# Performance work log

Measured on AMD Instinct MI355X. Metric: run time of the kernel, lower is better.

The kernel has to match this reference:

```python
import jax, jax.numpy as jnp
import numpy as np
import math

IN_DIM, ATTN_DIM, OUT_DIM, NUM_HEADS = 64, 128, 64, 4
B, N = 32, 1024


def setup_inputs() -> dict:
    key = jax.random.key(0)
    ks = jax.random.split(key, 8)
    def glorot(k, fan_in, fan_out):
        s = math.sqrt(6.0 / (fan_in + fan_out))
        return jax.random.uniform(k, (fan_in, fan_out), jnp.float32, -s, s)
    return {
        "x": jax.random.normal(ks[0], (B, N, IN_DIM), jnp.float32),
        "adj": jax.random.uniform(ks[1], (B, N, N), jnp.float32),
        "flags": jnp.ones((B, N), jnp.float32),
        "Wq": glorot(ks[2], IN_DIM, ATTN_DIM), "bq": jnp.zeros((ATTN_DIM,), jnp.float32),
        "Wk": glorot(ks[3], IN_DIM, ATTN_DIM), "bk": jnp.zeros((ATTN_DIM,), jnp.float32),
        "Wv": glorot(ks[4], IN_DIM, OUT_DIM), "bv": jnp.zeros((OUT_DIM,), jnp.float32),
    }


def dense_gcn(x, adj, W, b):
    # add self-loops (improved=False -> diagonal set to 1)
    n = adj.shape[-1]
    idx = jnp.arange(n)
    adj = adj.at[:, idx, idx].set(1.0)
    h = x @ W                                   # [B,N,C_out]
    d = jnp.clip(adj.sum(-1), 1.0) ** -0.5      # [B,N]
    adj_n = d[:, :, None] * adj * d[:, None, :]
    return adj_n @ h + b


def reference(x, adj, flags, Wq, bq, Wk, bk, Wv, bv):
    del flags  # accepted but unused by the original forward
    Q = dense_gcn(x, adj, Wq, bq)               # [B,N,attn]
    K = dense_gcn(x, adj, Wk, bk)               # [B,N,attn]
    V = dense_gcn(x, adj, Wv, bv)               # [B,N,out]
    dh = ATTN_DIM // NUM_HEADS
    b_, n_ = adj.shape[0], adj.shape[1]
    # torch.cat(split(dh,-1), dim=0) == heads as leading axis
    Q_ = Q.reshape(b_, n_, NUM_HEADS, dh).transpose(2, 0, 1, 3)  # [H,B,N,dh]
    K_ = K.reshape(b_, n_, NUM_HEADS, dh).transpose(2, 0, 1, 3)
    scores = jnp.einsum('hbnd,hbmd->hbnm', Q_, K_) / math.sqrt(OUT_DIM)
    A = jnp.tanh(scores)                        # [H,B,N,N]
    A = A.mean(axis=0)                          # [B,N,N]
    A = (A + A.transpose(0, 2, 1)) * 0.5        # symmetrize
    return V, A
```

## Files before the change

kernel.cpp:

```cpp
#include <hip/hip_runtime.h>
#include <stdint.h>

typedef __attribute__((ext_vector_type(4))) float f32x4;
typedef __attribute__((ext_vector_type(4))) unsigned int u32x4;
typedef __attribute__((ext_vector_type(2))) unsigned int u32x2;
typedef __attribute__((ext_vector_type(8))) short bf16x8;

__device__ __forceinline__ unsigned short f2bf(float f) {
    union { float f; unsigned int u; } c; c.f = f;
    unsigned int u = c.u;
    unsigned int r = (u + 0x7FFFu + ((u >> 16) & 1u)) >> 16;
    return (unsigned short)r;
}
__device__ __forceinline__ float bf2f(unsigned short h) {
    union { unsigned int u; float f; } c; c.u = ((unsigned int)h) << 16;
    return c.f;
}
__device__ __forceinline__ float tanh_fast(float x) {
    float t = __expf(2.0f * x);
    return 1.0f - 2.0f * __builtin_amdgcn_rcpf(t + 1.0f);
}

__global__ __launch_bounds__(256) void k_deg(const float* __restrict__ adj,
                                             float* __restrict__ dvec) {
    int wid = threadIdx.x >> 6, l = threadIdx.x & 63;
    int row = blockIdx.x * 4 + wid;
    int b = row >> 10, i = row & 1023;
    const float* rp = adj + ((size_t)b << 20) + ((size_t)i << 10);
    float s = 0.f;
#pragma unroll
    for (int it = 0; it < 4; ++it) {
        f32x4 v = *(const f32x4*)(rp + it * 256 + l * 4);
        s += v.x + v.y + v.z + v.w;
    }
#pragma unroll
    for (int m = 32; m >= 1; m >>= 1) s += __shfl_xor(s, m);
    if (l == 0) {
        float diag = rp[i];
        float S = s - diag + 1.0f;
        S = fmaxf(S, 1.0f);
        dvec[(b << 10) + i] = 1.0f / sqrtf(S);
    }
}

__global__ __launch_bounds__(256) void k_xs(const float* __restrict__ x,
                                            const float* __restrict__ dvec,
                                            unsigned short* __restrict__ xsT) {
    __shared__ float Lt[64][65];
    int b = blockIdx.x >> 4, j0 = (blockIdx.x & 15) << 6;
    int tid = threadIdx.x;
    {
        int r = tid >> 2, cseg = (tid & 3) << 4;
        float dj = dvec[(b << 10) + j0 + r];
        const float* xr = x + (((size_t)((b << 10) + j0 + r)) << 6) + cseg;
#pragma unroll
        for (int q = 0; q < 4; ++q) {
            f32x4 v = *(const f32x4*)(xr + (q << 2));
#pragma unroll
            for (int e = 0; e < 4; ++e) Lt[r][cseg + (q << 2) + e] = v[e] * dj;
        }
    }
    __syncthreads();
    {
        int c = tid >> 2, js = (tid & 3) << 4;
        unsigned int pk[8];
#pragma unroll
        for (int e = 0; e < 8; ++e) {
            unsigned short lo16 = f2bf(Lt[js + 2 * e][c]);
            unsigned short hi16 = f2bf(Lt[js + 2 * e + 1][c]);
            pk[e] = (unsigned)lo16 | ((unsigned)hi16 << 16);
        }
        unsigned short* op = xsT + ((size_t)b << 16) + ((size_t)c << 10) + j0 + js;
        u32x4 w0 = {pk[0], pk[1], pk[2], pk[3]};
        u32x4 w1 = {pk[4], pk[5], pk[6], pk[7]};
        *(u32x4*)op = w0;
        *(u32x4*)(op + 8) = w1;
    }
}

#define APAD 72
__global__ __launch_bounds__(256) void k_m(const float* __restrict__ adj,
                                           const unsigned short* __restrict__ xsT,
                                           const float* __restrict__ dvec,
                                           float* __restrict__ Mg) {
    __shared__ unsigned short Al[32][APAD];
    __shared__ unsigned short Bl[64][APAD];
    int bid = blockIdx.x;
    int xcd = bid & 7, t2 = bid >> 3;
    int bg = t2 >> 5, mt = t2 & 31;
    int b = (bg << 3) + xcd;
    int i0 = mt << 5;
    int tid = threadIdx.x;
    int wid = tid >> 6, l = tid & 63;
    int wm = wid >> 1, wn = wid & 1;
    int lr = l & 15, lg = l >> 4;

    f32x4 acc[2];
    acc[0] = (f32x4){0.f, 0.f, 0.f, 0.f};
    acc[1] = (f32x4){0.f, 0.f, 0.f, 0.f};

    const float* adjB = adj + ((size_t)b << 20);
    const unsigned short* xsB = xsT + ((size_t)b << 16);
    int ar0 = tid >> 4;
    int ac4 = (tid & 15) << 2;

    for (int kt = 0; kt < 16; ++kt) {
        int j0 = kt << 6;
        __syncthreads();
#pragma unroll
        for (int rr = 0; rr < 2; ++rr) {
            int row = ar0 + (rr << 4);
            int gi  = i0 + row;
            f32x4 v = *(const f32x4*)(adjB + ((size_t)gi << 10) + j0 + ac4);
            int gj = j0 + ac4;
            if (gj + 0 == gi) v.x = 1.0f;
            if (gj + 1 == gi) v.y = 1.0f;
            if (gj + 2 == gi) v.z = 1.0f;
            if (gj + 3 == gi) v.w = 1.0f;
            u32x2 pk;
            pk.x = (unsigned)f2bf(v.x) | ((unsigned)f2bf(v.y) << 16);
            pk.y = (unsigned)f2bf(v.z) | ((unsigned)f2bf(v.w) << 16);
            *(u32x2*)&Al[row][ac4] = pk;
        }
#pragma unroll
        for (int rep = 0; rep < 2; ++rep) {
            int idx = (rep << 8) + tid;
            int crow = idx >> 3, ch = (idx & 7) << 3;
            u32x4 v = *(const u32x4*)(xsB + ((size_t)crow << 10) + j0 + ch);
            *(u32x4*)&Bl[crow][ch] = v;
        }
        __syncthreads();
#pragma unroll
        for (int kk = 0; kk < 2; ++kk) {
            bf16x8 av = *(const bf16x8*)&Al[wm * 16 + lr][kk * 32 + lg * 8];
            bf16x8 b0 = *(const bf16x8*)&Bl[wn * 32 + lr][kk * 32 + lg * 8];
            bf16x8 b1 = *(const bf16x8*)&Bl[wn * 32 + 16 + lr][kk * 32 + lg * 8];
            acc[0] = __builtin_amdgcn_mfma_f32_16x16x32_bf16(av, b0, acc[0], 0, 0, 0);
            acc[1] = __builtin_amdgcn_mfma_f32_16x16x32_bf16(av, b1, acc[1], 0, 0, 0);
        }
    }
#pragma unroll
    for (int r = 0; r < 4; ++r) {
        int gi = i0 + wm * 16 + lg * 4 + r;
        float dv = dvec[(b << 10) + gi];
#pragma unroll
        for (int ni = 0; ni < 2; ++ni) {
            int cg = wn * 32 + ni * 16 + lr;
            Mg[(((size_t)((b << 10) + gi)) << 6) + cg] = dv * acc[ni][r];
        }
    }
}

#define QPAD 72
__global__ __launch_bounds__(256) void k_qkv(const float* __restrict__ Mg,
                                             const float* __restrict__ Wq,
                                             const float* __restrict__ Wk,
                                             const float* __restrict__ Wv,
                                             const float* __restrict__ bq,
                                             const float* __restrict__ bk,
                                             const float* __restrict__ bv,
                                             unsigned short* __restrict__ QKhi,
                                             unsigned short* __restrict__ QKlo,
                                             float* __restrict__ outV) {
    __shared__ unsigned short WThi[320][QPAD];
    __shared__ unsigned short WTlo[320][QPAD];
    __shared__ float biasl[320];
    int tid = threadIdx.x;
#pragma unroll 1
    for (int it = 0; it < 32; ++it) {
        int idx = (it << 8) + tid;
        int k = idx >> 7, c = idx & 127;
        float w = Wq[idx];
        unsigned short h = f2bf(w);
        WThi[c][k] = h; WTlo[c][k] = f2bf(w - bf2f(h));
    }
#pragma unroll 1
    for (int it = 0; it < 32; ++it) {
        int idx = (it << 8) + tid;
        int k = idx >> 7, c = idx & 127;
        float w = Wk[idx];
        unsigned short h = f2bf(w);
        WThi[128 + c][k] = h; WTlo[128 + c][k] = f2bf(w - bf2f(h));
    }
#pragma unroll 1
    for (int it = 0; it < 16; ++it) {
        int idx = (it << 8) + tid;
        int k = idx >> 6, c = idx & 63;
        float w = Wv[idx];
        unsigned short h = f2bf(w);
        WThi[256 + c][k] = h; WTlo[256 + c][k] = f2bf(w - bf2f(h));
    }
    for (int e = tid; e < 320; e += 256)
        biasl[e] = (e < 128) ? bq[e] : ((e < 256) ? bk[e - 128] : bv[e - 256]);

    int wid = tid >> 6, l = tid & 63, lr = l & 15, lg = l >> 4;
    int gr0 = (blockIdx.x << 6) + (wid << 4);
    const float* mrow = Mg + (((size_t)(gr0 + lr)) << 6);
    bf16x8 ahi[2], alo[2];
#pragma unroll
    for (int kk = 0; kk < 2; ++kk) {
        f32x4 v0 = *(const f32x4*)(mrow + kk * 32 + lg * 8);
        f32x4 v1 = *(const f32x4*)(mrow + kk * 32 + lg * 8 + 4);
#pragma unroll
        for (int e = 0; e < 8; ++e) {
            float f = (e < 4) ? v0[e] : v1[e - 4];
            unsigned short h = f2bf(f);
            ahi[kk][e] = (short)h;
            alo[kk][e] = (short)f2bf(f - bf2f(h));
        }
    }
    __syncthreads();

    f32x4 acc[20];
#pragma unroll
    for (int n = 0; n < 20; ++n) acc[n] = (f32x4){0.f, 0.f, 0.f, 0.f};
#pragma unroll
    for (int n = 0; n < 20; ++n) {
#pragma unroll
        for (int kk = 0; kk < 2; ++kk) {
            bf16x8 bh = *(const bf16x8*)&WThi[n * 16 + lr][kk * 32 + lg * 8];
            bf16x8 bl = *(const bf16x8*)&WTlo[n * 16 + lr][kk * 32 + lg * 8];
            acc[n] = __builtin_amdgcn_mfma_f32_16x16x32_bf16(ahi[kk], bh, acc[n], 0, 0, 0);
            acc[n] = __builtin_amdgcn_mfma_f32_16x16x32_bf16(ahi[kk], bl, acc[n], 0, 0, 0);
            acc[n] = __builtin_amdgcn_mfma_f32_16x16x32_bf16(alo[kk], bh, acc[n], 0, 0, 0);
        }
    }
#pragma unroll
    for (int n = 0; n < 20; ++n) {
        int c = n * 16 + lr;
        float bias = biasl[c];
#pragma unroll
        for (int r = 0; r < 4; ++r) {
            int gr = gr0 + lg * 4 + r;
            float val = acc[n][r] + bias;
            if (n < 16) {
                size_t base = ((size_t)gr << 8) + c;
                unsigned short h = f2bf(val);
                QKhi[base] = h;
                QKlo[base] = f2bf(val - bf2f(h));
            } else {
                outV[((size_t)gr << 6) + (c - 256)] = val;
            }
        }
    }
}

__global__ __launch_bounds__(256) void k_attn(const unsigned short* __restrict__ QKhi,
                                              const unsigned short* __restrict__ QKlo,
                                              float* __restrict__ Aout) {
    __shared__ float Sh[4][2][32][33];
    __shared__ float Asym[32][33];
    int bid = blockIdx.x;
    int xcd = bid & 7, t2 = bid >> 3;
    int bg = t2 / 528, pr = t2 - bg * 528;
    int b  = (bg << 3) + xcd;
    int ti = 0;
    {
        int p = pr;
        while (p >= (32 - ti)) { p -= (32 - ti); ++ti; }
        pr = p;
    }
    int tj = ti + pr;
    bool diag = (ti == tj);
    int qi0 = ti << 5, qj0 = tj << 5;
    int tid = threadIdx.x;
    int w = tid >> 6, l = tid & 63;
    int lr = l & 15, lg = l >> 4, lk = lg << 3;
    const unsigned short* hiB = QKhi + ((size_t)b << 18);
    const unsigned short* loB = QKlo + ((size_t)b << 18);
    int qcol = (w << 5) + lk;
    int kcol = 128 + (w << 5) + lk;

    {
        bf16x8 qh[2], ql[2], kh[2], kl[2];
#pragma unroll
        for (int m = 0; m < 2; ++m) {
            size_t off = ((size_t)(qi0 + (m << 4) + lr) << 8) + qcol;
            qh[m] = *(const bf16x8*)(hiB + off);
            ql[m] = *(const bf16x8*)(loB + off);
        }
#pragma unroll
        for (int n = 0; n < 2; ++n) {
            size_t off = ((size_t)(qj0 + (n << 4) + lr) << 8) + kcol;
            kh[n] = *(const bf16x8*)(hiB + off);
            kl[n] = *(const bf16x8*)(loB + off);
        }
#pragma unroll
        for (int m = 0; m < 2; ++m)
#pragma unroll
            for (int n = 0; n < 2; ++n) {
                f32x4 s = {0.f, 0.f, 0.f, 0.f};
                s = __builtin_amdgcn_mfma_f32_16x16x32_bf16(qh[m], kh[n], s, 0, 0, 0);
                s = __builtin_amdgcn_mfma_f32_16x16x32_bf16(qh[m], kl[n], s, 0, 0, 0);
                s = __builtin_amdgcn_mfma_f32_16x16x32_bf16(ql[m], kh[n], s, 0, 0, 0);
#pragma unroll
                for (int r = 0; r < 4; ++r)
                    Sh[w][0][(m << 4) + (lg << 2) + r][(n << 4) + lr] =
                        tanh_fast(s[r] * 0.125f);
            }
    }
    if (!diag) {
        bf16x8 qh[2], ql[2], kh[2], kl[2];
#pragma unroll
        for (int m = 0; m < 2; ++m) {
            size_t off = ((size_t)(qj0 + (m << 4) + lr) << 8) + qcol;
            qh[m] = *(const bf16x8*)(hiB + off);
            ql[m] = *(const bf16x8*)(loB + off);
        }
#pragma unroll
        for (int n = 0; n < 2; ++n) {
            size_t off = ((size_t)(qi0 + (n << 4) + lr) << 8) + kcol;
            kh[n] = *(const bf16x8*)(hiB + off);
            kl[n] = *(const bf16x8*)(loB + off);
        }
#pragma unroll
        for (int m = 0; m < 2; ++m)
#pragma unroll
            for (int n = 0; n < 2; ++n) {
                f32x4 s = {0.f, 0.f, 0.f, 0.f};
                s = __builtin_amdgcn_mfma_f32_16x16x32_bf16(qh[m], kh[n], s, 0, 0, 0);
                s = __builtin_amdgcn_mfma_f32_16x16x32_bf16(qh[m], kl[n], s, 0, 0, 0);
                s = __builtin_amdgcn_mfma_f32_16x16x32_bf16(ql[m], kh[n], s, 0, 0, 0);
#pragma unroll
                for (int r = 0; r < 4; ++r)
                    Sh[w][1][(m << 4) + (lg << 2) + r][(n << 4) + lr] =
                        tanh_fast(s[r] * 0.125f);
            }
    }
    __syncthreads();
    {
        int r = tid >> 3, c4 = (tid & 7) << 2;
        f32x4 v;
#pragma unroll
        for (int e = 0; e < 4; ++e) {
            int c = c4 + e;
            float tij = Sh[0][0][r][c] + Sh[1][0][r][c] + Sh[2][0][r][c] + Sh[3][0][r][c];
            float tji;
            if (diag) tji = Sh[0][0][c][r] + Sh[1][0][c][r] + Sh[2][0][c][r] + Sh[3][0][c][r];
            else      tji = Sh[0][1][c][r] + Sh[1][1][c][r] + Sh[2][1][c][r] + Sh[3][1][c][r];
            float a = 0.125f * (tij + tji);
            v[e] = a;
            Asym[r][c] = a;
        }
        *(f32x4*)(Aout + ((size_t)b << 20) + ((size_t)(qi0 + r) << 10) + qj0 + c4) = v;
    }
    if (!diag) {
        __syncthreads();
        int rj = tid >> 3, ci4 = (tid & 7) << 2;
        f32x4 v;
#pragma unroll
        for (int e = 0; e < 4; ++e) v[e] = Asym[ci4 + e][rj];
        *(f32x4*)(Aout + ((size_t)b << 20) + ((size_t)(qj0 + rj) << 10) + qi0 + ci4) = v;
    }
}

extern "C" void kernel_launch(void* const* d_in, const int* in_sizes, int n_in,
                              void* d_out, int out_size, void* d_ws, size_t ws_size,
                              hipStream_t stream) {
    const float* x   = (const float*)d_in[0];
    const float* adj = (const float*)d_in[1];
    const float* Wq = (const float*)d_in[3];
    const float* bq = (const float*)d_in[4];
    const float* Wk = (const float*)d_in[5];
    const float* bk = (const float*)d_in[6];
    const float* Wv = (const float*)d_in[7];
    const float* bv = (const float*)d_in[8];

    float* out  = (float*)d_out;
    float* outV = out;
    float* Aout = out + 2097152;

    char* ws = (char*)d_ws;
    float*          dvec = (float*)ws;
    unsigned short* xsT  = (unsigned short*)(ws + 131072);
    float*          Mg   = (float*)(ws + 131072 + 4194304);
    unsigned short* QKhi = (unsigned short*)(ws + 131072 + 4194304 + 8388608);
    unsigned short* QKlo = (unsigned short*)(ws + 131072 + 4194304 + 8388608 + 16777216);

    hipLaunchKernelGGL(k_deg,  dim3(8192),  dim3(256), 0, stream, adj, dvec);
    hipLaunchKernelGGL(k_xs,   dim3(512),   dim3(256), 0, stream, x, dvec, xsT);
    hipLaunchKernelGGL(k_m,    dim3(1024),  dim3(256), 0, stream, adj, xsT, dvec, Mg);
    hipLaunchKernelGGL(k_qkv,  dim3(512),   dim3(256), 0, stream, Mg, Wq, Wk, Wv,
                       bq, bk, bv, QKhi, QKlo, outV);
    hipLaunchKernelGGL(k_attn, dim3(16896), dim3(256), 0, stream, QKhi, QKlo, Aout);
}
```

Before: 418.7 us.

## Precompute split-bf16 weights once and restructure attention tile per-wave layout

The weight transpose and hi/lo bf16 split move out of k_qkv into one extra block of k_xs, which writes them to workspace. Each k_qkv block then does vectorized copies from that workspace instead of redoing the conversion 512 times. The attention kernel is reorganized so each wave owns a 16x16 sub-tile and loops over all four heads in registers, computing both S_ij and S_ji^T directly and summing tanh values in registers. This removes the large per-head shared-memory staging and one barrier, at the cost of more register loads (8 fragments per head) and doubled MFMA work on diagonal tiles.

```diff
diff --git a/kernel.cpp b/kernel.cpp
--- a/kernel.cpp
+++ b/kernel.cpp
@@ -45,10 +45,39 @@
 
 __global__ __launch_bounds__(256) void k_xs(const float* __restrict__ x,
                                             const float* __restrict__ dvec,
-                                            unsigned short* __restrict__ xsT) {
+                                            unsigned short* __restrict__ xsT,
+                                            const float* __restrict__ Wq,
+                                            const float* __restrict__ Wk,
+                                            const float* __restrict__ Wv,
+                                            const float* __restrict__ bq,
+                                            const float* __restrict__ bk,
+                                            const float* __restrict__ bv,
+                                            unsigned short* __restrict__ WThiG,
+                                            unsigned short* __restrict__ WTloG,
+                                            float* __restrict__ biasG) {
     __shared__ float Lt[64][65];
+    int tid = threadIdx.x;
+    if (blockIdx.x == 512) {
+        for (int idx = tid; idx < 8192; idx += 256) {
+            int k = idx >> 7, c = idx & 127;
+            float w = Wq[idx]; unsigned short h = f2bf(w);
+            WThiG[(c << 6) + k] = h; WTloG[(c << 6) + k] = f2bf(w - bf2f(h));
+        }
+        for (int idx = tid; idx < 8192; idx += 256) {
+            int k = idx >> 7, c = idx & 127;
+            float w = Wk[idx]; unsigned short h = f2bf(w);
+            WThiG[((128 + c) << 6) + k] = h; WTloG[((128 + c) << 6) + k] = f2bf(w - bf2f(h));
+        }
+        for (int idx = tid; idx < 4096; idx += 256) {
+            int k = idx >> 6, c = idx & 63;
+            float w = Wv[idx]; unsigned short h = f2bf(w);
+            WThiG[((256 + c) << 6) + k] = h; WTloG[((256 + c) << 6) + k] = f2bf(w - bf2f(h));
+        }
+        for (int e = tid; e < 320; e += 256)
+            biasG[e] = (e < 128) ? bq[e] : ((e < 256) ? bk[e - 128] : bv[e - 256]);
+        return;
+    }
     int b = blockIdx.x >> 4, j0 = (blockIdx.x & 15) << 6;
-    int tid = threadIdx.x;
     {
         int r = tid >> 2, cseg = (tid & 3) << 4;
         float dj = dvec[(b << 10) + j0 + r];
@@ -151,47 +180,25 @@
     }
 }
 
-#define QPAD 72
 __global__ __launch_bounds__(256) void k_qkv(const float* __restrict__ Mg,
-                                             const float* __restrict__ Wq,
-                                             const float* __restrict__ Wk,
-                                             const float* __restrict__ Wv,
-                                             const float* __restrict__ bq,
-                                             const float* __restrict__ bk,
-                                             const float* __restrict__ bv,
+                                             const unsigned short* __restrict__ WThiG,
+                                             const unsigned short* __restrict__ WTloG,
+                                             const float* __restrict__ biasG,
                                              unsigned short* __restrict__ QKhi,
                                              unsigned short* __restrict__ QKlo,
                                              float* __restrict__ outV) {
-    __shared__ unsigned short WThi[320][QPAD];
-    __shared__ unsigned short WTlo[320][QPAD];
+    __shared__ unsigned short WThi[320][72];
+    __shared__ unsigned short WTlo[320][72];
     __shared__ float biasl[320];
     int tid = threadIdx.x;
-#pragma unroll 1
-    for (int it = 0; it < 32; ++it) {
+#pragma unroll
+    for (int it = 0; it < 10; ++it) {
         int idx = (it << 8) + tid;
-        int k = idx >> 7, c = idx & 127;
-        float w = Wq[idx];
-        unsigned short h = f2bf(w);
-        WThi[c][k] = h; WTlo[c][k] = f2bf(w - bf2f(h));
-    }
-#pragma unroll 1
-    for (int it = 0; it < 32; ++it) {
-        int idx = (it << 8) + tid;
-        int k = idx >> 7, c = idx & 127;
-        float w = Wk[idx];
-        unsigned short h = f2bf(w);
-        WThi[128 + c][k] = h; WTlo[128 + c][k] = f2bf(w - bf2f(h));
-    }
-#pragma unroll 1
-    for (int it = 0; it < 16; ++it) {
-        int idx = (it << 8) + tid;
-        int k = idx >> 6, c = idx & 63;
-        float w = Wv[idx];
-        unsigned short h = f2bf(w);
-        WThi[256 + c][k] = h; WTlo[256 + c][k] = f2bf(w - bf2f(h));
-    }
-    for (int e = tid; e < 320; e += 256)
-        biasl[e] = (e < 128) ? bq[e] : ((e < 256) ? bk[e - 128] : bv[e - 256]);
+        int row = idx >> 3, cs = (idx & 7) << 3;
+        *(u32x4*)&WThi[row][cs] = *(const u32x4*)(WThiG + (row << 6) + cs);
+        *(u32x4*)&WTlo[row][cs] = *(const u32x4*)(WTloG + (row << 6) + cs);
+    }
+    for (int e = tid; e < 320; e += 256) biasl[e] = biasG[e];
 
     int wid = tid >> 6, l = tid & 63, lr = l & 15, lg = l >> 4;
     int gr0 = (blockIdx.x << 6) + (wid << 4);
@@ -248,109 +255,67 @@
 __global__ __launch_bounds__(256) void k_attn(const unsigned short* __restrict__ QKhi,
                                               const unsigned short* __restrict__ QKlo,
                                               float* __restrict__ Aout) {
-    __shared__ float Sh[4][2][32][33];
-    __shared__ float Asym[32][33];
+    __shared__ float As[32][36];
     int bid = blockIdx.x;
     int xcd = bid & 7, t2 = bid >> 3;
     int bg = t2 / 528, pr = t2 - bg * 528;
     int b  = (bg << 3) + xcd;
     int ti = 0;
-    {
-        int p = pr;
-        while (p >= (32 - ti)) { p -= (32 - ti); ++ti; }
-        pr = p;
-    }
+    { int p = pr; while (p >= (32 - ti)) { p -= (32 - ti); ++ti; } pr = p; }
     int tj = ti + pr;
     bool diag = (ti == tj);
     int qi0 = ti << 5, qj0 = tj << 5;
     int tid = threadIdx.x;
-    int w = tid >> 6, l = tid & 63;
-    int lr = l & 15, lg = l >> 4, lk = lg << 3;
+    int wid = tid >> 6, l = tid & 63;
+    int wm = wid >> 1, wn = wid & 1;
+    int lr = l & 15, lg = l >> 4, ko = lg << 3;
     const unsigned short* hiB = QKhi + ((size_t)b << 18);
     const unsigned short* loB = QKlo + ((size_t)b << 18);
-    int qcol = (w << 5) + lk;
-    int kcol = 128 + (w << 5) + lk;
-
-    {
-        bf16x8 qh[2], ql[2], kh[2], kl[2];
-#pragma unroll
-        for (int m = 0; m < 2; ++m) {
-            size_t off = ((size_t)(qi0 + (m << 4) + lr) << 8) + qcol;
-            qh[m] = *(const bf16x8*)(hiB + off);
-            ql[m] = *(const bf16x8*)(loB + off);
-        }
-#pragma unroll
-        for (int n = 0; n < 2; ++n) {
-            size_t off = ((size_t)(qj0 + (n << 4) + lr) << 8) + kcol;
-            kh[n] = *(const bf16x8*)(hiB + off);
-            kl[n] = *(const bf16x8*)(loB + off);
-        }
-#pragma unroll
-        for (int m = 0; m < 2; ++m)
-#pragma unroll
-            for (int n = 0; n < 2; ++n) {
-                f32x4 s = {0.f, 0.f, 0.f, 0.f};
-                s = __builtin_amdgcn_mfma_f32_16x16x32_bf16(qh[m], kh[n], s, 0, 0, 0);
-                s = __builtin_amdgcn_mfma_f32_16x16x32_bf16(qh[m], kl[n], s, 0, 0, 0);
-                s = __builtin_amdgcn_mfma_f32_16x16x32_bf16(ql[m], kh[n], s, 0, 0, 0);
-#pragma unroll
-                for (int r = 0; r < 4; ++r)
-                    Sh[w][0][(m << 4) + (lg << 2) + r][(n << 4) + lr] =
-                        tanh_fast(s[r] * 0.125f);
-            }
-    }
+    size_t offI = ((size_t)(qi0 + wm * 16 + lr) << 8) + ko;
+    size_t offJ = ((size_t)(qj0 + wn * 16 + lr) << 8) + ko;
+
+    bf16x8 qih[4], qil[4], kih[4], kil[4], kjh[4], kjl[4], qjh[4], qjl[4];
+#pragma unroll
+    for (int h = 0; h < 4; ++h) {
+        int hq = h << 5;
+        int hk = 128 + (h << 5);
+        qih[h] = *(const bf16x8*)(hiB + offI + hq);
+        qil[h] = *(const bf16x8*)(loB + offI + hq);
+        kih[h] = *(const bf16x8*)(hiB + offI + hk);
+        kil[h] = *(const bf16x8*)(loB + offI + hk);
+        kjh[h] = *(const bf16x8*)(hiB + offJ + hk);
+        kjl[h] = *(const bf16x8*)(loB + offJ + hk);
+        qjh[h] = *(const bf16x8*)(hiB + offJ + hq);
+        qjl[h] = *(const bf16x8*)(loB + offJ + hq);
+    }
+    f32x4 asum = {0.f, 0.f, 0.f, 0.f};
+#pragma unroll
+    for (int h = 0; h < 4; ++h) {
+        f32x4 s0 = {0.f, 0.f, 0.f, 0.f}, s1 = {0.f, 0.f, 0.f, 0.f};
+        s0 = __builtin_amdgcn_mfma_f32_16x16x32_bf16(qih[h], kjh[h], s0, 0, 0, 0);
+        s0 = __builtin_amdgcn_mfma_f32_16x16x32_bf16(qih[h], kjl[h], s0, 0, 0, 0);
+        s0 = __builtin_amdgcn_mfma_f32_16x16x32_bf16(qil[h], kjh[h], s0, 0, 0, 0);
+        s1 = __builtin_amdgcn_mfma_f32_16x16x32_bf16(kih[h], qjh[h], s1, 0, 0, 0);
+        s1 = __builtin_amdgcn_mfma_f32_16x16x32_bf16(kih[h], qjl[h], s1, 0, 0, 0);
+        s1 = __builtin_amdgcn_mfma_f32_16x16x32_bf16(kil[h], qjh[h], s1, 0, 0, 0);
+#pragma unroll
+        for (int r = 0; r < 4; ++r)
+            asum[r] += tanh_fast(s0[r] * 0.125f) + tanh_fast(s1[r] * 0.125f);
+    }
+#pragma unroll
+    for (int r = 0; r < 4; ++r)
+        As[wm * 16 + (lg << 2) + r][wn * 16 + lr] = asum[r] * 0.125f;
+    __syncthreads();
+    int row = tid >> 3, c4 = (tid & 7) << 2;
+    f32x4 v;
+#pragma unroll
+    for (int e = 0; e < 4; ++e) v[e] = As[row][c4 + e];
+    *(f32x4*)(Aout + ((size_t)b << 20) + ((size_t)(qi0 + row) << 10) + qj0 + c4) = v;
     if (!diag) {
-        bf16x8 qh[2], ql[2], kh[2], kl[2];
-#pragma unroll
-        for (int m = 0; m < 2; ++m) {
-            size_t off = ((size_t)(qj0 + (m << 4) + lr) << 8) + qcol;
-            qh[m] = *(const bf16x8*)(hiB + off);
-            ql[m] = *(const bf16x8*)(loB + off);
-        }
-#pragma unroll
-        for (int n = 0; n < 2; ++n) {
-            size_t off = ((size_t)(qi0 + (n << 4) + lr) << 8) + kcol;
-            kh[n] = *(const bf16x8*)(hiB + off);
-            kl[n] = *(const bf16x8*)(loB + off);
-        }
-#pragma unroll
-        for (int m = 0; m < 2; ++m)
-#pragma unroll
-            for (int n = 0; n < 2; ++n) {
-                f32x4 s = {0.f, 0.f, 0.f, 0.f};
-                s = __builtin_amdgcn_mfma_f32_16x16x32_bf16(qh[m], kh[n], s, 0, 0, 0);
-                s = __builtin_amdgcn_mfma_f32_16x16x32_bf16(qh[m], kl[n], s, 0, 0, 0);
-                s = __builtin_amdgcn_mfma_f32_16x16x32_bf16(ql[m], kh[n], s, 0, 0, 0);
-#pragma unroll
-                for (int r = 0; r < 4; ++r)
-                    Sh[w][1][(m << 4) + (lg << 2) + r][(n << 4) + lr] =
-                        tanh_fast(s[r] * 0.125f);
-            }
-    }
-    __syncthreads();
-    {
-        int r = tid >> 3, c4 = (tid & 7) << 2;
-        f32x4 v;
-#pragma unroll
-        for (int e = 0; e < 4; ++e) {
-            int c = c4 + e;
-            float tij = Sh[0][0][r][c] + Sh[1][0][r][c] + Sh[2][0][r][c] + Sh[3][0][r][c];
-            float tji;
-            if (diag) tji = Sh[0][0][c][r] + Sh[1][0][c][r] + Sh[2][0][c][r] + Sh[3][0][c][r];
-            else      tji = Sh[0][1][c][r] + Sh[1][1][c][r] + Sh[2][1][c][r] + Sh[3][1][c][r];
-            float a = 0.125f * (tij + tji);
-            v[e] = a;
-            Asym[r][c] = a;
-        }
-        *(f32x4*)(Aout + ((size_t)b << 20) + ((size_t)(qi0 + r) << 10) + qj0 + c4) = v;
-    }
-    if (!diag) {
-        __syncthreads();
-        int rj = tid >> 3, ci4 = (tid & 7) << 2;
-        f32x4 v;
-#pragma unroll
-        for (int e = 0; e < 4; ++e) v[e] = Asym[ci4 + e][rj];
-        *(f32x4*)(Aout + ((size_t)b << 20) + ((size_t)(qj0 + rj) << 10) + qi0 + ci4) = v;
+        f32x4 w2;
+#pragma unroll
+        for (int e = 0; e < 4; ++e) w2[e] = As[c4 + e][row];
+        *(f32x4*)(Aout + ((size_t)b << 20) + ((size_t)(qj0 + row) << 10) + qi0 + c4) = w2;
     }
 }
 
@@ -371,16 +336,20 @@
     float* Aout = out + 2097152;
 
     char* ws = (char*)d_ws;
-    float*          dvec = (float*)ws;
-    unsigned short* xsT  = (unsigned short*)(ws + 131072);
-    float*          Mg   = (float*)(ws + 131072 + 4194304);
-    unsigned short* QKhi = (unsigned short*)(ws + 131072 + 4194304 + 8388608);
-    unsigned short* QKlo = (unsigned short*)(ws + 131072 + 4194304 + 8388608 + 16777216);
+    float*          dvec  = (float*)ws;
+    unsigned short* xsT   = (unsigned short*)(ws + 131072);
+    float*          Mg    = (float*)(ws + 4325376);
+    unsigned short* QKhi  = (unsigned short*)(ws + 12713984);
+    unsigned short* QKlo  = (unsigned short*)(ws + 29491200);
+    unsigned short* WThiG = (unsigned short*)(ws + 46268416);
+    unsigned short* WTloG = (unsigned short*)(ws + 46309376);
+    float*          biasG = (float*)(ws + 46350336);
 
     hipLaunchKernelGGL(k_deg,  dim3(8192),  dim3(256), 0, stream, adj, dvec);
-    hipLaunchKernelGGL(k_xs,   dim3(512),   dim3(256), 0, stream, x, dvec, xsT);
+    hipLaunchKernelGGL(k_xs,   dim3(513),   dim3(256), 0, stream, x, dvec, xsT,
+                       Wq, Wk, Wv, bq, bk, bv, WThiG, WTloG, biasG);
     hipLaunchKernelGGL(k_m,    dim3(1024),  dim3(256), 0, stream, adj, xsT, dvec, Mg);
-    hipLaunchKernelGGL(k_qkv,  dim3(512),   dim3(256), 0, stream, Mg, Wq, Wk, Wv,
-                       bq, bk, bv, QKhi, QKlo, outV);
+    hipLaunchKernelGGL(k_qkv,  dim3(512),   dim3(256), 0, stream, Mg, WThiG, WTloG,
+                       biasG, QKhi, QKlo, outV);
     hipLaunchKernelGGL(k_attn, dim3(16896), dim3(256), 0, stream, QKhi, QKlo, Aout);
 }
```

After: 565.2 us. 35.0% more time.
